# Kernel optimization log

Measured on AMD Instinct MI355X. Metric: run time of the kernel, lower is better.

The kernel has to match this reference:

```python
import jax, jax.numpy as jnp
import numpy as np

N_E = 8192
SPLIT = (512, 512)
BETA = 0.25
ENTROPY_RATIO = 0.1
TEMPERATURE = 0.01


def _l2norm(x):
    return x / jnp.linalg.norm(x, axis=-1, keepdims=True)


def _pairwise_sq_dist(zf, emb):
    # ||z||^2 + ||e||^2 - 2 z @ e^T   -> [N, n_e]
    return (jnp.sum(zf ** 2, axis=1, keepdims=True)
            + jnp.sum(emb ** 2, axis=1)
            - 2.0 * jnp.einsum('bd,nd->bn', zf, emb))


def _entropy_loss(affinity):
    flat = affinity / TEMPERATURE                      # [N, n_e]
    probs = jax.nn.softmax(flat, axis=-1)
    log_probs = jax.nn.log_softmax(flat + 1e-5, axis=-1)
    avg_probs = jnp.mean(probs, axis=0)                # [n_e]
    avg_entropy = -jnp.sum(avg_probs * jnp.log(avg_probs + 1e-5))
    sample_entropy = -jnp.mean(jnp.sum(probs * log_probs, axis=-1))
    return sample_entropy - avg_entropy


def setup_inputs() -> dict:
    key = jax.random.key(0)
    k1, k2, k3 = jax.random.split(key, 3)
    z = jax.random.normal(k1, (8192, 1024), dtype=jnp.float32)
    lim = 1.0 / N_E
    emb_text = jax.random.uniform(k2, (N_E, SPLIT[0]), minval=-lim, maxval=lim, dtype=jnp.float32)
    emb_graph = jax.random.uniform(k3, (N_E, SPLIT[1]), minval=-lim, maxval=lim, dtype=jnp.float32)
    # l2_norm=True: codebook weights are normalized at init
    emb_text = _l2norm(emb_text)
    emb_graph = _l2norm(emb_graph)
    return {"z": z, "emb_text": emb_text, "emb_graph": emb_graph}


def reference(z, emb_text, emb_graph):
    st = SPLIT[0]
    z_text, z_graph = z[:, :st], z[:, st:]

    # l2_norm path: normalize inputs and codebooks
    zt = _l2norm(z_text)                               # [N, d_t]
    zg = _l2norm(z_graph)                              # [N, d_g]
    et = _l2norm(emb_text)                             # [n_e, d_t]
    eg = _l2norm(emb_graph)                            # [n_e, d_g]
    z_norm = jnp.concatenate([zt, zg], axis=-1)        # [N, e_dim]

    d_text = _pairwise_sq_dist(zt, et)                 # [N, n_e]
    d_graph = _pairwise_sq_dist(zg, eg)                # [N, n_e]
    text_d_norm = jnp.mean(jnp.sum(d_text ** 2, axis=-1))
    graph_d_norm = jnp.mean(jnp.sum(d_graph ** 2, axis=-1))

    d = d_text + 1.0 * d_graph
    min_encoding_indices = jnp.argmin(d, axis=1)       # [N]

    all_embedding = jnp.concatenate([et, eg], axis=-1) # [n_e, e_dim]
    z_q = all_embedding[min_encoding_indices]          # [N, e_dim]
    z_q_text = et[min_encoding_indices]
    z_q_graph = eg[min_encoding_indices]

    sg = jax.lax.stop_gradient
    vq_loss = jnp.mean((z_q - sg(z_norm)) ** 2)
    commit_loss = BETA * jnp.mean((sg(z_q) - z_norm) ** 2)
    entropy_loss = ENTROPY_RATIO * _entropy_loss(-d)

    z_q_out = z_norm + sg(z_q - z_norm)                # straight-through
    return (z_q_out, vq_loss, commit_loss, entropy_loss,
            text_d_norm, graph_d_norm, z_q_text, z_q_graph,
            min_encoding_indices)
```

## Files before the change

### kernel.cpp

```cpp
#include <hip/hip_runtime.h>
#include <cmath>

using f32x4 = __attribute__((ext_vector_type(4))) float;
using f16x8 = __attribute__((ext_vector_type(8))) _Float16;

#define SCL_H  256.0f
#define INV_HH (1.0f/65536.0f)

#define WS_ZH   ((size_t)0)
#define WS_ZL   ((size_t)4194304)
#define WS_EH   ((size_t)8388608)
#define WS_EL   ((size_t)12582912)
#define WS_Z2T  ((size_t)16777216)
#define WS_Z2G  ((size_t)16785408)
#define WS_E2T  ((size_t)16793600)
#define WS_E2G  ((size_t)16801792)
#define WS_PM   ((size_t)16809984)
#define WS_PZ   ((size_t)17334272)
#define WS_PS1  ((size_t)17858560)
#define WS_PDT  ((size_t)18382848)
#define WS_PDG  ((size_t)18907136)
#define WS_PD1  ((size_t)19431424)
#define WS_PD2  ((size_t)19955712)
#define WS_PI1  ((size_t)20480000)
#define WS_PI2  ((size_t)21004288)
#define WS_PSC  ((size_t)21528576)
#define WS_LSE  ((size_t)22052864)
#define WS_IDX  ((size_t)22061056)
#define WS_RENT ((size_t)22069248)
#define WS_RDT  ((size_t)22077440)
#define WS_RDG  ((size_t)22085632)
#define WS_GVQ  ((size_t)22093824)
#define WS_AVG4 ((size_t)22102016)
#define WS_QM   ((size_t)22167552)
#define WS_STORE_END ((size_t)55721984)

#define O_VQ  ((size_t)8388608)
#define O_CM  ((size_t)8388609)
#define O_ENT ((size_t)8388610)
#define O_TD  ((size_t)8388611)
#define O_GD  ((size_t)8388612)
#define O_ZT  ((size_t)8388613)
#define O_ZG  ((size_t)12582917)
#define O_IX  ((size_t)16777221)

__device__ __forceinline__ size_t tiled_off(int row, int chunk) {
    return (((size_t)(row >> 7) * 32 + (chunk >> 2)) * 4 + (size_t)(chunk & 3)) * 1024
           + (size_t)(row & 127) * 8;
}

__device__ __forceinline__ void gload16(const void* g, void* l) {
    __builtin_amdgcn_global_load_lds(
        (const __attribute__((address_space(1))) unsigned int*)g,
        (__attribute__((address_space(3))) unsigned int*)l, 16, 0, 0);
}

__device__ __forceinline__ f32x4 mfma16(f16x8 a, f16x8 b, f32x4 c) {
    return __builtin_amdgcn_mfma_f32_16x16x32_f16(a, b, c, 0, 0, 0);
}

__device__ __forceinline__ unsigned short f2bf(float x) {
    unsigned int u = __float_as_uint(x);
    return (unsigned short)((u + 0x7fffu + ((u >> 16) & 1u)) >> 16);
}
__device__ __forceinline__ float bf2f(unsigned short u) {
    return __uint_as_float(((unsigned int)u) << 16);
}

__device__ __forceinline__ bool dless(float a, int ia, float b, int ib) {
    return a < b || (a == b && ia < ib);
}
__device__ __forceinline__ void top2_point(float& d1, int& i1, float& d2, int& i2,
                                           float d, int j) {
    if (dless(d, j, d1, i1)) { d2 = d1; i2 = i1; d1 = d; i1 = j; }
    else if (dless(d, j, d2, i2)) { d2 = d; i2 = j; }
}
__device__ __forceinline__ void top2_merge(float& d1, int& i1, float& d2, int& i2,
                                           float od1, int oi1, float od2, int oi2) {
    if (dless(od1, oi1, d1, i1)) {
        float nd2; int ni2;
        if (dless(d1, i1, od2, oi2)) { nd2 = d1; ni2 = i1; } else { nd2 = od2; ni2 = oi2; }
        d1 = od1; i1 = oi1; d2 = nd2; i2 = ni2;
    } else if (dless(od1, oi1, d2, i2)) {
        d2 = od1; i2 = oi1;
    }
}

__global__ __launch_bounds__(256) void k_zero(float* __restrict__ p, int n) {
    int i = blockIdx.x * 256 + threadIdx.x;
    if (i < n) p[i] = 0.0f;
}

__global__ __launch_bounds__(1024) void k_norm_z(const float* __restrict__ z,
        _Float16* __restrict__ zh, _Float16* __restrict__ zl,
        float* __restrict__ z2t, float* __restrict__ z2g) {
    int t = threadIdx.x;
    int r8 = t & 7, ck = t >> 3;
    int row = blockIdx.x * 8 + r8;
    const float* src = z + (size_t)row * 1024 + (size_t)ck * 8;
    float4 v0 = *(const float4*)src;
    float4 v1 = *(const float4*)(src + 4);
    float v[8] = {v0.x,v0.y,v0.z,v0.w,v1.x,v1.y,v1.z,v1.w};
    float ss = 0.f;
#pragma unroll
    for (int e = 0; e < 8; ++e) ss += v[e]*v[e];
    __shared__ float red[8*132];
    int ri = r8*132 + ck;
    red[ri] = ss; __syncthreads();
    for (int s = 32; s > 0; s >>= 1) { if ((ck & 63) < s) red[ri] += red[ri+s]; __syncthreads(); }
    float nrm = sqrtf(red[r8*132 + (ck & 64)]);
    float nv[8]; float s2 = 0.f;
#pragma unroll
    for (int e = 0; e < 8; ++e) { nv[e] = v[e]/nrm; s2 += nv[e]*nv[e]; }
    __syncthreads();
    red[ri] = s2; __syncthreads();
    for (int s = 32; s > 0; s >>= 1) { if ((ck & 63) < s) red[ri] += red[ri+s]; __syncthreads(); }
    if ((ck & 63) == 0) { if (ck & 64) z2g[row] = red[ri]; else z2t[row] = red[ri]; }
    f16x8 h8, l8;
#pragma unroll
    for (int e = 0; e < 8; ++e) {
        float xs = nv[e]*SCL_H;
        _Float16 h = (_Float16)xs; h8[e] = h;
        l8[e] = (_Float16)((xs - (float)h) * 4096.0f);
    }
    size_t off = tiled_off(row, ck);
    *(f16x8*)(zh + off) = h8;
    *(f16x8*)(zl + off) = l8;
}

__global__ __launch_bounds__(1024) void k_norm_e(const float* __restrict__ et, const float* __restrict__ eg,
        _Float16* __restrict__ eh, _Float16* __restrict__ el,
        float* __restrict__ e2t, float* __restrict__ e2g) {
    int t = threadIdx.x;
    int r8 = t & 7, ck = t >> 3;
    int row = blockIdx.x * 8 + r8;
    const float* src = (ck < 64) ? (et + (size_t)row * 512 + (size_t)ck * 8)
                                 : (eg + (size_t)row * 512 + (size_t)(ck - 64) * 8);
    float4 v0 = *(const float4*)src;
    float4 v1 = *(const float4*)(src + 4);
    float v[8] = {v0.x,v0.y,v0.z,v0.w,v1.x,v1.y,v1.z,v1.w};
    float ss = 0.f;
#pragma unroll
    for (int e = 0; e < 8; ++e) ss += v[e]*v[e];
    __shared__ float red[8*132];
    int ri = r8*132 + ck;
    red[ri] = ss; __syncthreads();
    for (int s = 32; s > 0; s >>= 1) { if ((ck & 63) < s) red[ri] += red[ri+s]; __syncthreads(); }
    float nrm = sqrtf(red[r8*132 + (ck & 64)]);
    float nv[8]; float s2 = 0.f;
#pragma unroll
    for (int e = 0; e < 8; ++e) { nv[e] = v[e]/nrm; s2 += nv[e]*nv[e]; }
    __syncthreads();
    red[ri] = s2; __syncthreads();
    for (int s = 32; s > 0; s >>= 1) { if ((ck & 63) < s) red[ri] += red[ri+s]; __syncthreads(); }
    if ((ck & 63) == 0) { if (ck & 64) e2g[row] = red[ri]; else e2t[row] = red[ri]; }
    f16x8 h8, l8;
#pragma unroll
    for (int e = 0; e < 8; ++e) {
        float xs = nv[e]*SCL_H;
        _Float16 h = (_Float16)xs; h8[e] = h;
        l8[e] = (_Float16)((xs - (float)h) * 4096.0f);
    }
    size_t off = tiled_off(row, ck);
    *(f16x8*)(eh + off) = h8;
    *(f16x8*)(el + off) = l8;
}

template<int PASS, bool STOREQ>
__global__ __launch_bounds__(512, 2) void k_gemm(
    const _Float16* __restrict__ zht, const _Float16* __restrict__ eht,
    const float* __restrict__ z2t, const float* __restrict__ z2g,
    const float* __restrict__ e2t, const float* __restrict__ e2g,
    float* __restrict__ pm, float* __restrict__ pz, float* __restrict__ ps1,
    float* __restrict__ pdt, float* __restrict__ pdg,
    float* __restrict__ pd1, float* __restrict__ pd2,
    int* __restrict__ pi1, int* __restrict__ pi2,
    unsigned short* __restrict__ qm,
    const float* __restrict__ lse, float* __restrict__ avgp)
{
    const int nj = blockIdx.x, bi = blockIdx.y;
    const int t = threadIdx.x;
    const int lane = t & 63, wid = t >> 6;
    const int wave_r = wid >> 2, wave_c = wid & 3;
    const int jf = lane & 15, g = lane >> 4;

    __shared__ __align__(16) _Float16 stg[2][2][4096];
    __shared__ float sM[128][4], sDt[128][4], sDg[128][4], sZ[128][4], sS1[128][4];
    __shared__ float sD1[128][4], sD2[128][4];
    __shared__ int   sI1[128][4], sI2[128][4];
    __shared__ float sMf[128];
    __shared__ float scol[128];

    if (PASS == 2 && t < 128) scol[t] = 0.f;

    f32x4 acct[4][2] = {};
    f32x4 accg[4][2] = {};

    const _Float16* pa = zht + (size_t)bi * 131072 + (size_t)t * 8;
    const _Float16* pb = eht + (size_t)nj * 131072 + (size_t)t * 8;

#define STAGE(KT, B) { \
        gload16(pa + (size_t)(KT) * 4096, &stg[0][B][t * 8]); \
        gload16(pb + (size_t)(KT) * 4096, &stg[1][B][t * 8]); }

    int cur = 0;
    STAGE(0, 0)
    asm volatile("s_waitcnt vmcnt(0)" ::: "memory");
    __syncthreads();

    for (int kt = 0; kt < 32; ++kt) {
        if (kt + 1 < 32) {
            if (cur == 0) STAGE(kt + 1, 1) else STAGE(kt + 1, 0)
        }
        f16x8 ah[4], bh[2];
#pragma unroll
        for (int fr = 0; fr < 4; ++fr) {
            int off = g * 1024 + (wave_r * 64 + fr * 16 + jf) * 8;
            ah[fr] = *(const f16x8*)&stg[0][cur][off];
        }
#pragma unroll
        for (int fc = 0; fc < 2; ++fc) {
            int off = g * 1024 + (wave_c * 32 + fc * 16 + jf) * 8;
            bh[fc] = *(const f16x8*)&stg[1][cur][off];
        }
        if (kt < 16) {
#pragma unroll
            for (int fr = 0; fr < 4; ++fr)
#pragma unroll
            for (int fc = 0; fc < 2; ++fc)
                acct[fr][fc] = mfma16(ah[fr], bh[fc], acct[fr][fc]);
        } else {
#pragma unroll
            for (int fr = 0; fr < 4; ++fr)
#pragma unroll
            for (int fc = 0; fc < 2; ++fc)
                accg[fr][fc] = mfma16(ah[fr], bh[fc], accg[fr][fc]);
        }
        asm volatile("s_waitcnt vmcnt(0)" ::: "memory");
        __syncthreads();
        cur ^= 1;
    }
#undef STAGE

    const int colbase = nj * 128 + wave_c * 32;
    float e2tc[2], e2gc[2];
#pragma unroll
    for (int fc = 0; fc < 2; ++fc) {
        e2tc[fc] = e2t[colbase + fc * 16 + jf];
        e2gc[fc] = e2g[colbase + fc * 16 + jf];
    }

    if constexpr (PASS == 1) {
#pragma unroll
        for (int fr = 0; fr < 4; ++fr) {
#pragma unroll
            for (int reg = 0; reg < 4; ++reg) {
                int rl = wave_r * 64 + fr * 16 + g * 4 + reg;
                int i  = bi * 128 + rl;
                float z2ti = z2t[i], z2gi = z2g[i];
                float mrow = -3.0e38f, dt2 = 0.f, dg2 = 0.f;
                float d1 = 3.0e38f, d2 = 3.0e38f;
                int i1 = 0x7fffffff, i2 = 0x7fffffff;
#pragma unroll
                for (int fc = 0; fc < 2; ++fc) {
                    float ht = acct[fr][fc][reg], hg = accg[fr][fc][reg];
                    float dta = z2ti + e2tc[fc] - ht * (2.0f * INV_HH);
                    float dga = z2gi + e2gc[fc] - hg * (2.0f * INV_HH);
                    float d   = dta + dga;
                    float lv  = -100.0f * d;
                    acct[fr][fc][reg] = lv;
                    dt2 += dta * dta; dg2 += dga * dga;
                    int j = colbase + fc * 16 + jf;
                    top2_point(d1, i1, d2, i2, d, j);
                    mrow = fmaxf(mrow, lv);
                }
#pragma unroll
                for (int s = 1; s < 16; s <<= 1) {
                    mrow = fmaxf(mrow, __shfl_xor(mrow, s));
                    dt2 += __shfl_xor(dt2, s);
                    dg2 += __shfl_xor(dg2, s);
                    float od1 = __shfl_xor(d1, s); int oi1 = __shfl_xor(i1, s);
                    float od2 = __shfl_xor(d2, s); int oi2 = __shfl_xor(i2, s);
                    top2_merge(d1, i1, d2, i2, od1, oi1, od2, oi2);
                }
                if (jf == 0) {
                    sM[rl][wave_c] = mrow; sDt[rl][wave_c] = dt2; sDg[rl][wave_c] = dg2;
                    sD1[rl][wave_c] = d1; sI1[rl][wave_c] = i1;
                    sD2[rl][wave_c] = d2; sI2[rl][wave_c] = i2;
                }
            }
        }
        __syncthreads();
        if (t < 128) sMf[t] = fmaxf(fmaxf(sM[t][0], sM[t][1]), fmaxf(sM[t][2], sM[t][3]));
        __syncthreads();
#pragma unroll
        for (int fr = 0; fr < 4; ++fr) {
#pragma unroll
            for (int reg = 0; reg < 4; ++reg) {
                int rl = wave_r * 64 + fr * 16 + g * 4 + reg;
                float M = sMf[rl];
                float Z = 0.f, S1 = 0.f;
#pragma unroll
                for (int fc = 0; fc < 2; ++fc) {
                    float lv = acct[fr][fc][reg];
                    float e  = expf(lv - M);
                    Z += e; S1 += e * lv;
                    if constexpr (STOREQ) {
                        size_t qo = (size_t)(bi * 128 + rl) * 8192 + (colbase + fc * 16 + jf);
                        qm[qo] = f2bf(e);
                    }
                }
#pragma unroll
                for (int s = 1; s < 16; s <<= 1) {
                    Z  += __shfl_xor(Z, s);
                    S1 += __shfl_xor(S1, s);
                }
                if (jf == 0) { sZ[rl][wave_c] = Z; sS1[rl][wave_c] = S1; }
            }
        }
        __syncthreads();
        if (t < 128) {
            float M = sMf[t];
            float Z = sZ[t][0] + sZ[t][1] + sZ[t][2] + sZ[t][3];
            float S1 = sS1[t][0] + sS1[t][1] + sS1[t][2] + sS1[t][3];
            float dt2 = sDt[t][0] + sDt[t][1] + sDt[t][2] + sDt[t][3];
            float dg2 = sDg[t][0] + sDg[t][1] + sDg[t][2] + sDg[t][3];
            float d1 = sD1[t][0], d2 = sD2[t][0];
            int i1 = sI1[t][0], i2 = sI2[t][0];
#pragma unroll
            for (int w = 1; w < 4; ++w)
                top2_merge(d1, i1, d2, i2, sD1[t][w], sI1[t][w], sD2[t][w], sI2[t][w]);
            size_t pb = (size_t)(bi * 128 + t) * 64 + nj;
            pm[pb] = M; pz[pb] = Z; ps1[pb] = S1;
            pdt[pb] = dt2; pdg[pb] = dg2;
            pd1[pb] = d1; pd2[pb] = d2; pi1[pb] = i1; pi2[pb] = i2;
        }
    } else {
        float cs0 = 0.f, cs1 = 0.f;
#pragma unroll
        for (int fr = 0; fr < 4; ++fr) {
#pragma unroll
            for (int reg = 0; reg < 4; ++reg) {
                int rl = wave_r * 64 + fr * 16 + g * 4 + reg;
                int i  = bi * 128 + rl;
                float z2ti = z2t[i], z2gi = z2g[i];
                float lsei = lse[i];
#pragma unroll
                for (int fc = 0; fc < 2; ++fc) {
                    float ht = acct[fr][fc][reg], hg = accg[fr][fc][reg];
                    float d = (z2ti + z2gi) + (e2tc[fc] + e2gc[fc])
                            - 2.0f * INV_HH * (ht + hg);
                    float lv = -100.0f * d;
                    float p = expf(lv - lsei);
                    if (fc == 0) cs0 += p; else cs1 += p;
                }
            }
        }
        cs0 += __shfl_xor(cs0, 16); cs0 += __shfl_xor(cs0, 32);
        cs1 += __shfl_xor(cs1, 16); cs1 += __shfl_xor(cs1, 32);
        if (g == 0) {
            atomicAdd(&scol[wave_c * 32 + jf], cs0);
            atomicAdd(&scol[wave_c * 32 + 16 + jf], cs1);
        }
        __syncthreads();
        if (t < 128) atomicAdd(&avgp[nj * 128 + t], scol[t]);
    }
}

__global__ __launch_bounds__(256) void k_rowreduce(
    const float* __restrict__ pm, const float* __restrict__ pz, const float* __restrict__ ps1,
    const float* __restrict__ pdt, const float* __restrict__ pdg,
    float* __restrict__ pscale, float* __restrict__ lse,
    float* __restrict__ rent, float* __restrict__ rdt, float* __restrict__ rdg)
{
    int b = blockIdx.x * 4 + (threadIdx.x >> 6);
    int l = threadIdx.x & 63;
    size_t pb = (size_t)b * 64 + l;
    float m0 = pm[pb];
    float m = m0;
#pragma unroll
    for (int s = 1; s < 64; s <<= 1) m = fmaxf(m, __shfl_xor(m, s));
    float sc = expf(m0 - m);
    float Z = pz[pb] * sc, S1 = ps1[pb] * sc;
    float dt2 = pdt[pb], dg2 = pdg[pb];
#pragma unroll
    for (int s = 1; s < 64; s <<= 1) {
        Z += __shfl_xor(Z, s); S1 += __shfl_xor(S1, s);
        dt2 += __shfl_xor(dt2, s); dg2 += __shfl_xor(dg2, s);
    }
    float lseb = m + logf(Z);
    pscale[pb] = expf(m0 - lseb);
    if (l == 0) {
        lse[b] = lseb;
        rent[b] = lseb - S1 / Z;
        rdt[b] = dt2; rdg[b] = dg2;
    }
}

__global__ __launch_bounds__(256) void k_refine(
    const float* __restrict__ pd1, const float* __restrict__ pd2,
    const int* __restrict__ pi1, const int* __restrict__ pi2,
    const _Float16* __restrict__ zh, const _Float16* __restrict__ zl,
    const _Float16* __restrict__ eh, const _Float16* __restrict__ el,
    const float* __restrict__ z2t, const float* __restrict__ z2g,
    const float* __restrict__ e2t, const float* __restrict__ e2g,
    int* __restrict__ idxi, float* __restrict__ out)
{
    int row = blockIdx.x * 4 + (threadIdx.x >> 6);
    int l = threadIdx.x & 63;
    size_t base = (size_t)row * 64;
    float da = pd1[base + l]; int ja = pi1[base + l];
    float db = pd2[base + l]; int jb = pi2[base + l];
    float M = fminf(da, db);
#pragma unroll
    for (int s = 1; s < 64; s <<= 1) M = fminf(M, __shfl_xor(M, s));
    const float eps = 1.0e-3f;
    unsigned long long mA = __ballot(da <= M + eps);
    unsigned long long mB = __ballot(db <= M + eps);

    float zv[16];
    {
        size_t o0 = tiled_off(row, 2 * l), o1 = tiled_off(row, 2 * l + 1);
        f16x8 h0 = *(const f16x8*)(zh + o0), l0 = *(const f16x8*)(zl + o0);
        f16x8 h1 = *(const f16x8*)(zh + o1), l1 = *(const f16x8*)(zl + o1);
#pragma unroll
        for (int e = 0; e < 8; ++e) {
            zv[e]     = (float)h0[e] * (1.0f/256.0f) + (float)l0[e] * (1.0f/1048576.0f);
            zv[8 + e] = (float)h1[e] * (1.0f/256.0f) + (float)l1[e] * (1.0f/1048576.0f);
        }
    }
    float zz = z2t[row] + z2g[row];
    float bd = 3.0e38f; int bj = 0x7fffffff;
    while (mA | mB) {
        int cand;
        if (mA) { int s = (int)__ffsll(mA) - 1; mA &= mA - 1; cand = __shfl(ja, s); }
        else    { int s = (int)__ffsll(mB) - 1; mB &= mB - 1; cand = __shfl(jb, s); }
        size_t o0 = tiled_off(cand, 2 * l), o1 = tiled_off(cand, 2 * l + 1);
        f16x8 h0 = *(const f16x8*)(eh + o0), l0 = *(const f16x8*)(el + o0);
        f16x8 h1 = *(const f16x8*)(eh + o1), l1 = *(const f16x8*)(el + o1);
        float dot = 0.f;
#pragma unroll
        for (int e = 0; e < 8; ++e) {
            float ev0 = (float)h0[e] * (1.0f/256.0f) + (float)l0[e] * (1.0f/1048576.0f);
            float ev1 = (float)h1[e] * (1.0f/256.0f) + (float)l1[e] * (1.0f/1048576.0f);
            dot += zv[e] * ev0 + zv[8 + e] * ev1;
        }
#pragma unroll
        for (int s = 1; s < 64; s <<= 1) dot += __shfl_xor(dot, s);
        float d = zz + e2t[cand] + e2g[cand] - 2.0f * dot;
        if (d < bd || (d == bd && cand < bj)) { bd = d; bj = cand; }
    }
    if (l == 0) { idxi[row] = bj; out[O_IX + row] = (float)bj; }
}

__global__ __launch_bounds__(256) void k_colsum(const unsigned short* __restrict__ qm,
                                                const float* __restrict__ pscale,
                                                float* __restrict__ avg4) {
    int cc = blockIdx.x, rb = blockIdx.y, t = threadIdx.x;
    int cp = t & 63, rg = t >> 6;
    float a0 = 0.f, a1 = 0.f;
    const unsigned short* qb = qm + (size_t)cc * 128 + (size_t)cp * 2;
#pragma unroll 4
    for (int rr = rg; rr < 1024; rr += 4) {
        int r = rb * 1024 + rr;
        float s = pscale[(size_t)r * 64 + cc];
        unsigned int q = *(const unsigned int*)(qb + (size_t)r * 8192);
        a0 += bf2f((unsigned short)(q & 0xffffu)) * s;
        a1 += bf2f((unsigned short)(q >> 16)) * s;
    }
    __shared__ float red[512];
    red[rg * 128 + cp * 2] = a0; red[rg * 128 + cp * 2 + 1] = a1;
    __syncthreads();
    if (rg == 0) {
        float s0 = red[cp*2]   + red[128+cp*2]   + red[256+cp*2]   + red[384+cp*2];
        float s1 = red[cp*2+1] + red[128+cp*2+1] + red[256+cp*2+1] + red[384+cp*2+1];
        avg4[(size_t)rb * 8192 + cc * 128 + cp * 2]     = s0;
        avg4[(size_t)rb * 8192 + cc * 128 + cp * 2 + 1] = s1;
    }
}

__global__ __launch_bounds__(1024) void k_gather(
    const _Float16* __restrict__ zh, const _Float16* __restrict__ zl,
    const _Float16* __restrict__ eh, const _Float16* __restrict__ el,
    const int* __restrict__ idxi, float* __restrict__ out, float* __restrict__ gvq)
{
    int t = threadIdx.x;
    int r8 = t & 7, ck = t >> 3;
    int b = blockIdx.x * 8 + r8;
    int idx = idxi[b];
    size_t zo = tiled_off(b, ck), eo = tiled_off(idx, ck);
    f16x8 zh8 = *(const f16x8*)(zh + zo);
    f16x8 zl8 = *(const f16x8*)(zl + zo);
    f16x8 eh8 = *(const f16x8*)(eh + eo);
    f16x8 el8 = *(const f16x8*)(el + eo);
    float ss = 0.f; float oz[8], zq[8];
#pragma unroll
    for (int e = 0; e < 8; ++e) {
        float zn = ((float)zh8[e] + (float)zl8[e] * (1.0f / 4096.0f)) * (1.0f / SCL_H);
        float eq = ((float)eh8[e] + (float)el8[e] * (1.0f / 4096.0f)) * (1.0f / SCL_H);
        float df = eq - zn;
        zq[e] = eq; oz[e] = zn + df; ss += df * df;
    }
    float* dst = out + (size_t)b * 1024 + (size_t)ck * 8;
    *(float4*)dst       = make_float4(oz[0], oz[1], oz[2], oz[3]);
    *(float4*)(dst + 4) = make_float4(oz[4], oz[5], oz[6], oz[7]);
    float* tg = (ck < 64) ? (out + O_ZT + (size_t)b * 512 + (size_t)ck * 8)
                          : (out + O_ZG + (size_t)b * 512 + (size_t)(ck - 64) * 8);
    *(float4*)tg       = make_float4(zq[0], zq[1], zq[2], zq[3]);
    *(float4*)(tg + 4) = make_float4(zq[4], zq[5], zq[6], zq[7]);
    __shared__ float red[8*132];
    int ri = r8 * 132 + ck;
    red[ri] = ss; __syncthreads();
    for (int s = 64; s > 0; s >>= 1) { if (ck < s) red[ri] += red[ri + s]; __syncthreads(); }
    if (ck == 0) gvq[b] = red[ri];
}

__global__ __launch_bounds__(256) void k_finalize(const float* __restrict__ avg4,
        const float* __restrict__ rent, const float* __restrict__ rdt,
        const float* __restrict__ rdg, const float* __restrict__ gvq,
        float* __restrict__ out) {
    int t = threadIdx.x;
    float ent = 0.f, se = 0.f, dt = 0.f, dg = 0.f, vq = 0.f;
    for (int n = t; n < 8192; n += 256) {
        float a = 0.f;
#pragma unroll
        for (int k = 0; k < 8; ++k) a += avg4[(size_t)k * 8192 + n];
        a *= (1.0f / 8192.0f);
        ent -= a * logf(a + 1e-5f);
        se += rent[n]; dt += rdt[n]; dg += rdg[n]; vq += gvq[n];
    }
    __shared__ float red[256];
#define RED(x) { red[t] = x; __syncthreads(); \
    for (int s = 128; s > 0; s >>= 1) { if (t < s) red[t] += red[t + s]; __syncthreads(); } \
    x = red[0]; __syncthreads(); }
    RED(ent) RED(se) RED(dt) RED(dg) RED(vq)
#undef RED
    if (t == 0) {
        float vqm = vq * (1.0f / 8388608.0f);
        out[O_VQ]  = vqm;
        out[O_CM]  = 0.25f * vqm;
        out[O_ENT] = 0.1f * (se * (1.0f / 8192.0f) - ent);
        out[O_TD]  = dt * (1.0f / 8192.0f);
        out[O_GD]  = dg * (1.0f / 8192.0f);
    }
}

extern "C" void kernel_launch(void* const* d_in, const int* in_sizes, int n_in,
                              void* d_out, int out_size, void* d_ws, size_t ws_size,
                              hipStream_t stream) {
    const float* z  = (const float*)d_in[0];
    const float* et = (const float*)d_in[1];
    const float* eg = (const float*)d_in[2];
    float* out = (float*)d_out;
    float* ws  = (float*)d_ws;

    _Float16* zh = (_Float16*)(ws + WS_ZH);
    _Float16* zl = (_Float16*)(ws + WS_ZL);
    _Float16* eh = (_Float16*)(ws + WS_EH);
    _Float16* el = (_Float16*)(ws + WS_EL);
    float* z2t = ws + WS_Z2T;
    float* z2g = ws + WS_Z2G;
    float* e2t = ws + WS_E2T;
    float* e2g = ws + WS_E2G;
    float* pm  = ws + WS_PM;
    float* pz  = ws + WS_PZ;
    float* ps1 = ws + WS_PS1;
    float* pdt = ws + WS_PDT;
    float* pdg = ws + WS_PDG;
    float* pd1 = ws + WS_PD1;
    float* pd2 = ws + WS_PD2;
    int*   pi1 = (int*)(ws + WS_PI1);
    int*   pi2 = (int*)(ws + WS_PI2);
    float* psc = ws + WS_PSC;
    float* lsep = ws + WS_LSE;
    int*   idxi = (int*)(ws + WS_IDX);
    float* rent = ws + WS_RENT;
    float* rdt  = ws + WS_RDT;
    float* rdg  = ws + WS_RDG;
    float* gvq  = ws + WS_GVQ;
    float* avg4 = ws + WS_AVG4;
    unsigned short* qm = (unsigned short*)(ws + WS_QM);

    bool storeq = (ws_size >= WS_STORE_END * sizeof(float));

    k_norm_z<<<1024, 1024, 0, stream>>>(z, zh, zl, z2t, z2g);
    k_norm_e<<<1024, 1024, 0, stream>>>(et, eg, eh, el, e2t, e2g);

    dim3 gg(64, 64);
    if (storeq) {
        k_gemm<1, true><<<gg, 512, 0, stream>>>(zh, eh, z2t, z2g, e2t, e2g,
                                                pm, pz, ps1, pdt, pdg,
                                                pd1, pd2, pi1, pi2, qm, lsep, avg4);
    } else {
        k_gemm<1, false><<<gg, 512, 0, stream>>>(zh, eh, z2t, z2g, e2t, e2g,
                                                 pm, pz, ps1, pdt, pdg,
                                                 pd1, pd2, pi1, pi2, qm, lsep, avg4);
    }
    k_rowreduce<<<2048, 256, 0, stream>>>(pm, pz, ps1, pdt, pdg,
                                          psc, lsep, rent, rdt, rdg);
    k_refine<<<2048, 256, 0, stream>>>(pd1, pd2, pi1, pi2, zh, zl, eh, el,
                                       z2t, z2g, e2t, e2g, idxi, out);
    if (storeq) {
        k_colsum<<<dim3(64, 8), 256, 0, stream>>>(qm, psc, avg4);
    } else {
        k_zero<<<256, 256, 0, stream>>>(avg4, 65536);
        k_gemm<2, false><<<gg, 512, 0, stream>>>(zh, eh, z2t, z2g, e2t, e2g,
                                                 pm, pz, ps1, pdt, pdg,
                                                 pd1, pd2, pi1, pi2, qm, lsep, avg4);
    }
    k_gather<<<1024, 1024, 0, stream>>>(zh, zl, eh, el, idxi, out, gvq);
    k_finalize<<<1, 256, 0, stream>>>(avg4, rent, rdt, rdg, gvq, out);
}
```

Measured before the change: 801.3 us.

## Shrink GEMM tile to 128x64 with XCD-aware block mapping and LDS-staged Q stores

Reworks the fused distance GEMM to use 256-thread blocks computing 128x64 tiles, with a 1D grid remapped so that blocks sharing the same z row-tile land on the same XCD for L2 reuse. The K loop now takes 64-wide chunks per step with a single LDS buffer instead of double buffering. The bf16 probability matrix is staged through LDS and written with coalesced 16-byte stores instead of scattered 2-byte ones. Partial-result arrays double to 128 per row, so the row-reduce, refine (now with four candidate sets and a wider eps) and colsum kernels are adjusted, which adds more partial traffic and more candidate rescoring.

```diff
diff --git a/kernel.cpp b/kernel.cpp
--- a/kernel.cpp
+++ b/kernel.cpp
@@ -16,24 +16,24 @@
 #define WS_E2T  ((size_t)16793600)
 #define WS_E2G  ((size_t)16801792)
 #define WS_PM   ((size_t)16809984)
-#define WS_PZ   ((size_t)17334272)
-#define WS_PS1  ((size_t)17858560)
-#define WS_PDT  ((size_t)18382848)
-#define WS_PDG  ((size_t)18907136)
-#define WS_PD1  ((size_t)19431424)
-#define WS_PD2  ((size_t)19955712)
-#define WS_PI1  ((size_t)20480000)
-#define WS_PI2  ((size_t)21004288)
-#define WS_PSC  ((size_t)21528576)
-#define WS_LSE  ((size_t)22052864)
-#define WS_IDX  ((size_t)22061056)
-#define WS_RENT ((size_t)22069248)
-#define WS_RDT  ((size_t)22077440)
-#define WS_RDG  ((size_t)22085632)
-#define WS_GVQ  ((size_t)22093824)
-#define WS_AVG4 ((size_t)22102016)
-#define WS_QM   ((size_t)22167552)
-#define WS_STORE_END ((size_t)55721984)
+#define WS_PZ   ((size_t)17858560)
+#define WS_PS1  ((size_t)18907136)
+#define WS_PDT  ((size_t)19955712)
+#define WS_PDG  ((size_t)21004288)
+#define WS_PD1  ((size_t)22052864)
+#define WS_PD2  ((size_t)23101440)
+#define WS_PI1  ((size_t)24150016)
+#define WS_PI2  ((size_t)25198592)
+#define WS_PSC  ((size_t)26247168)
+#define WS_LSE  ((size_t)27295744)
+#define WS_IDX  ((size_t)27303936)
+#define WS_RENT ((size_t)27312128)
+#define WS_RDT  ((size_t)27320320)
+#define WS_RDG  ((size_t)27328512)
+#define WS_GVQ  ((size_t)27336704)
+#define WS_AVG4 ((size_t)27344896)
+#define WS_QM   ((size_t)27418624)
+#define WS_STORE_END ((size_t)60973056)
 
 #define O_VQ  ((size_t)8388608)
 #define O_CM  ((size_t)8388609)
@@ -167,7 +167,7 @@
 }
 
 template<int PASS, bool STOREQ>
-__global__ __launch_bounds__(512, 2) void k_gemm(
+__global__ __launch_bounds__(256, 4) void k_gemm(
     const _Float16* __restrict__ zht, const _Float16* __restrict__ eht,
     const float* __restrict__ z2t, const float* __restrict__ z2g,
     const float* __restrict__ e2t, const float* __restrict__ e2g,
@@ -178,71 +178,88 @@
     unsigned short* __restrict__ qm,
     const float* __restrict__ lse, float* __restrict__ avgp)
 {
-    const int nj = blockIdx.x, bi = blockIdx.y;
+    const int bid = blockIdx.x;
+    const int xcd = bid & 7, local = bid >> 3;
+    const int nj = local >> 3;
+    const int bi = xcd * 8 + (local & 7);
+
     const int t = threadIdx.x;
     const int lane = t & 63, wid = t >> 6;
-    const int wave_r = wid >> 2, wave_c = wid & 3;
+    const int wave_r = wid >> 1, wave_c = wid & 1;
     const int jf = lane & 15, g = lane >> 4;
 
-    __shared__ __align__(16) _Float16 stg[2][2][4096];
-    __shared__ float sM[128][4], sDt[128][4], sDg[128][4], sZ[128][4], sS1[128][4];
-    __shared__ float sD1[128][4], sD2[128][4];
-    __shared__ int   sI1[128][4], sI2[128][4];
-    __shared__ float sMf[128];
-    __shared__ float scol[128];
-
-    if (PASS == 2 && t < 128) scol[t] = 0.f;
+    __shared__ __align__(16) char smem[35328];
+    _Float16* lA = (_Float16*)smem;
+    _Float16* lB = (_Float16*)(smem + 16384);
+    unsigned short* sQ = (unsigned short*)smem;
+    float (*sM)[2]  = (float(*)[2])(smem + 24576);
+    float (*sDt)[2] = (float(*)[2])(smem + 25600);
+    float (*sDg)[2] = (float(*)[2])(smem + 26624);
+    float (*sZ)[2]  = (float(*)[2])(smem + 27648);
+    float (*sS1)[2] = (float(*)[2])(smem + 28672);
+    float (*sD1)[2] = (float(*)[2])(smem + 29696);
+    float (*sD2)[2] = (float(*)[2])(smem + 30720);
+    int   (*sI1)[2] = (int(*)[2])(smem + 31744);
+    int   (*sI2)[2] = (int(*)[2])(smem + 32768);
+    float* sMf  = (float*)(smem + 33792);
+    float* scol = (float*)(smem + 34304);
+
+    if (PASS == 2 && t < 64) scol[t] = 0.f;
 
     f32x4 acct[4][2] = {};
     f32x4 accg[4][2] = {};
 
-    const _Float16* pa = zht + (size_t)bi * 131072 + (size_t)t * 8;
-    const _Float16* pb = eht + (size_t)nj * 131072 + (size_t)t * 8;
-
-#define STAGE(KT, B) { \
-        gload16(pa + (size_t)(KT) * 4096, &stg[0][B][t * 8]); \
-        gload16(pb + (size_t)(KT) * 4096, &stg[1][B][t * 8]); }
-
-    int cur = 0;
-    STAGE(0, 0)
-    asm volatile("s_waitcnt vmcnt(0)" ::: "memory");
-    __syncthreads();
-
-    for (int kt = 0; kt < 32; ++kt) {
-        if (kt + 1 < 32) {
-            if (cur == 0) STAGE(kt + 1, 1) else STAGE(kt + 1, 0)
-        }
-        f16x8 ah[4], bh[2];
-#pragma unroll
-        for (int fr = 0; fr < 4; ++fr) {
-            int off = g * 1024 + (wave_r * 64 + fr * 16 + jf) * 8;
-            ah[fr] = *(const f16x8*)&stg[0][cur][off];
-        }
-#pragma unroll
-        for (int fc = 0; fc < 2; ++fc) {
-            int off = g * 1024 + (wave_c * 32 + fc * 16 + jf) * 8;
-            bh[fc] = *(const f16x8*)&stg[1][cur][off];
-        }
-        if (kt < 16) {
-#pragma unroll
-            for (int fr = 0; fr < 4; ++fr)
-#pragma unroll
-            for (int fc = 0; fc < 2; ++fc)
-                acct[fr][fc] = mfma16(ah[fr], bh[fc], acct[fr][fc]);
-        } else {
-#pragma unroll
-            for (int fr = 0; fr < 4; ++fr)
-#pragma unroll
-            for (int fc = 0; fc < 2; ++fc)
-                accg[fr][fc] = mfma16(ah[fr], bh[fc], accg[fr][fc]);
-        }
+    const _Float16* pa  = zht + (size_t)bi * 131072;
+    const _Float16* pbv = eht + (size_t)(nj >> 1) * 131072 + (size_t)(nj & 1) * 512;
+
+#define STAGE(KT2) { \
+        size_t kofs = (size_t)(KT2) * 8192; \
+        gload16(pa + kofs + (size_t)t * 8,         lA + t * 8); \
+        gload16(pa + kofs + (size_t)(256 + t) * 8, lA + (256 + t) * 8); \
+        gload16(pa + kofs + (size_t)(512 + t) * 8, lA + (512 + t) * 8); \
+        gload16(pa + kofs + (size_t)(768 + t) * 8, lA + (768 + t) * 8); \
+        { int li = t;       gload16(pbv + kofs + (size_t)(li >> 6) * 1024 + (size_t)(li & 63) * 8, lB + li * 8); } \
+        { int li = 256 + t; gload16(pbv + kofs + (size_t)(li >> 6) * 1024 + (size_t)(li & 63) * 8, lB + li * 8); } }
+
+    for (int kt2 = 0; kt2 < 16; ++kt2) {
+        STAGE(kt2)
         asm volatile("s_waitcnt vmcnt(0)" ::: "memory");
         __syncthreads();
-        cur ^= 1;
+        f16x8 a0[4], a1[4], b0[2], b1[2];
+#pragma unroll
+        for (int fr = 0; fr < 4; ++fr) {
+            int ro = (wave_r * 64 + fr * 16 + jf) * 8;
+            a0[fr] = *(const f16x8*)&lA[g * 1024 + ro];
+            a1[fr] = *(const f16x8*)&lA[4096 + g * 1024 + ro];
+        }
+#pragma unroll
+        for (int fc = 0; fc < 2; ++fc) {
+            int ro = (wave_c * 32 + fc * 16 + jf) * 8;
+            b0[fc] = *(const f16x8*)&lB[g * 512 + ro];
+            b1[fc] = *(const f16x8*)&lB[2048 + g * 512 + ro];
+        }
+        if (kt2 < 8) {
+#pragma unroll
+            for (int fr = 0; fr < 4; ++fr)
+#pragma unroll
+            for (int fc = 0; fc < 2; ++fc) {
+                acct[fr][fc] = mfma16(a0[fr], b0[fc], acct[fr][fc]);
+                acct[fr][fc] = mfma16(a1[fr], b1[fc], acct[fr][fc]);
+            }
+        } else {
+#pragma unroll
+            for (int fr = 0; fr < 4; ++fr)
+#pragma unroll
+            for (int fc = 0; fc < 2; ++fc) {
+                accg[fr][fc] = mfma16(a0[fr], b0[fc], accg[fr][fc]);
+                accg[fr][fc] = mfma16(a1[fr], b1[fc], accg[fr][fc]);
+            }
+        }
+        __syncthreads();
     }
 #undef STAGE
 
-    const int colbase = nj * 128 + wave_c * 32;
+    const int colbase = nj * 64 + wave_c * 32;
     float e2tc[2], e2gc[2];
 #pragma unroll
     for (int fc = 0; fc < 2; ++fc) {
@@ -291,7 +308,7 @@
             }
         }
         __syncthreads();
-        if (t < 128) sMf[t] = fmaxf(fmaxf(sM[t][0], sM[t][1]), fmaxf(sM[t][2], sM[t][3]));
+        if (t < 128) sMf[t] = fmaxf(sM[t][0], sM[t][1]);
         __syncthreads();
 #pragma unroll
         for (int fr = 0; fr < 4; ++fr) {
@@ -305,10 +322,7 @@
                     float lv = acct[fr][fc][reg];
                     float e  = expf(lv - M);
                     Z += e; S1 += e * lv;
-                    if constexpr (STOREQ) {
-                        size_t qo = (size_t)(bi * 128 + rl) * 8192 + (colbase + fc * 16 + jf);
-                        qm[qo] = f2bf(e);
-                    }
+                    if constexpr (STOREQ) sQ[rl * 64 + wave_c * 32 + fc * 16 + jf] = f2bf(e);
                 }
 #pragma unroll
                 for (int s = 1; s < 16; s <<= 1) {
@@ -321,19 +335,27 @@
         __syncthreads();
         if (t < 128) {
             float M = sMf[t];
-            float Z = sZ[t][0] + sZ[t][1] + sZ[t][2] + sZ[t][3];
-            float S1 = sS1[t][0] + sS1[t][1] + sS1[t][2] + sS1[t][3];
-            float dt2 = sDt[t][0] + sDt[t][1] + sDt[t][2] + sDt[t][3];
-            float dg2 = sDg[t][0] + sDg[t][1] + sDg[t][2] + sDg[t][3];
+            float Z = sZ[t][0] + sZ[t][1];
+            float S1 = sS1[t][0] + sS1[t][1];
+            float dt2 = sDt[t][0] + sDt[t][1];
+            float dg2 = sDg[t][0] + sDg[t][1];
             float d1 = sD1[t][0], d2 = sD2[t][0];
             int i1 = sI1[t][0], i2 = sI2[t][0];
-#pragma unroll
-            for (int w = 1; w < 4; ++w)
-                top2_merge(d1, i1, d2, i2, sD1[t][w], sI1[t][w], sD2[t][w], sI2[t][w]);
-            size_t pb = (size_t)(bi * 128 + t) * 64 + nj;
+            top2_merge(d1, i1, d2, i2, sD1[t][1], sI1[t][1], sD2[t][1], sI2[t][1]);
+            size_t pb = (size_t)(bi * 128 + t) * 128 + nj;
             pm[pb] = M; pz[pb] = Z; ps1[pb] = S1;
             pdt[pb] = dt2; pdg[pb] = dg2;
             pd1[pb] = d1; pd2[pb] = d2; pi1[pb] = i1; pi2[pb] = i2;
+        }
+        if constexpr (STOREQ) {
+            const uint4* s4 = (const uint4*)sQ;
+#pragma unroll
+            for (int it = 0; it < 4; ++it) {
+                int f = it * 256 + t;
+                int row = f >> 3, seg = f & 7;
+                uint4 q = s4[f];
+                *(uint4*)(qm + (size_t)(bi * 128 + row) * 8192 + nj * 64 + seg * 8) = q;
+            }
         }
     } else {
         float cs0 = 0.f, cs1 = 0.f;
@@ -363,7 +385,7 @@
             atomicAdd(&scol[wave_c * 32 + 16 + jf], cs1);
         }
         __syncthreads();
-        if (t < 128) atomicAdd(&avgp[nj * 128 + t], scol[t]);
+        if (t < 64) atomicAdd(&avgp[nj * 64 + t], scol[t]);
     }
 }
 
@@ -375,21 +397,23 @@
 {
     int b = blockIdx.x * 4 + (threadIdx.x >> 6);
     int l = threadIdx.x & 63;
-    size_t pb = (size_t)b * 64 + l;
-    float m0 = pm[pb];
-    float m = m0;
+    size_t i0 = (size_t)b * 128 + l, i1 = i0 + 64;
+    float ma = pm[i0], mb = pm[i1];
+    float m = fmaxf(ma, mb);
 #pragma unroll
     for (int s = 1; s < 64; s <<= 1) m = fmaxf(m, __shfl_xor(m, s));
-    float sc = expf(m0 - m);
-    float Z = pz[pb] * sc, S1 = ps1[pb] * sc;
-    float dt2 = pdt[pb], dg2 = pdg[pb];
+    float sa = expf(ma - m), sb = expf(mb - m);
+    float Z  = pz[i0] * sa + pz[i1] * sb;
+    float S1 = ps1[i0] * sa + ps1[i1] * sb;
+    float dt2 = pdt[i0] + pdt[i1], dg2 = pdg[i0] + pdg[i1];
 #pragma unroll
     for (int s = 1; s < 64; s <<= 1) {
         Z += __shfl_xor(Z, s); S1 += __shfl_xor(S1, s);
         dt2 += __shfl_xor(dt2, s); dg2 += __shfl_xor(dg2, s);
     }
     float lseb = m + logf(Z);
-    pscale[pb] = expf(m0 - lseb);
+    pscale[i0] = expf(ma - lseb);
+    pscale[i1] = expf(mb - lseb);
     if (l == 0) {
         lse[b] = lseb;
         rent[b] = lseb - S1 / Z;
@@ -408,15 +432,19 @@
 {
     int row = blockIdx.x * 4 + (threadIdx.x >> 6);
     int l = threadIdx.x & 63;
-    size_t base = (size_t)row * 64;
-    float da = pd1[base + l]; int ja = pi1[base + l];
-    float db = pd2[base + l]; int jb = pi2[base + l];
-    float M = fminf(da, db);
+    size_t base = (size_t)row * 128;
+    float cd[4]; int ci[4];
+    cd[0] = pd1[base + l];      ci[0] = pi1[base + l];
+    cd[1] = pd1[base + 64 + l]; ci[1] = pi1[base + 64 + l];
+    cd[2] = pd2[base + l];      ci[2] = pi2[base + l];
+    cd[3] = pd2[base + 64 + l]; ci[3] = pi2[base + 64 + l];
+    float M = fminf(fminf(cd[0], cd[1]), fminf(cd[2], cd[3]));
 #pragma unroll
     for (int s = 1; s < 64; s <<= 1) M = fminf(M, __shfl_xor(M, s));
-    const float eps = 1.0e-3f;
-    unsigned long long mA = __ballot(da <= M + eps);
-    unsigned long long mB = __ballot(db <= M + eps);
+    const float eps = 4.0e-3f;
+    unsigned long long mk[4];
+#pragma unroll
+    for (int k = 0; k < 4; ++k) mk[k] = __ballot(cd[k] <= M + eps);
 
     float zv[16];
     {
@@ -431,24 +459,26 @@
     }
     float zz = z2t[row] + z2g[row];
     float bd = 3.0e38f; int bj = 0x7fffffff;
-    while (mA | mB) {
-        int cand;
-        if (mA) { int s = (int)__ffsll(mA) - 1; mA &= mA - 1; cand = __shfl(ja, s); }
-        else    { int s = (int)__ffsll(mB) - 1; mB &= mB - 1; cand = __shfl(jb, s); }
-        size_t o0 = tiled_off(cand, 2 * l), o1 = tiled_off(cand, 2 * l + 1);
-        f16x8 h0 = *(const f16x8*)(eh + o0), l0 = *(const f16x8*)(el + o0);
-        f16x8 h1 = *(const f16x8*)(eh + o1), l1 = *(const f16x8*)(el + o1);
-        float dot = 0.f;
-#pragma unroll
-        for (int e = 0; e < 8; ++e) {
-            float ev0 = (float)h0[e] * (1.0f/256.0f) + (float)l0[e] * (1.0f/1048576.0f);
-            float ev1 = (float)h1[e] * (1.0f/256.0f) + (float)l1[e] * (1.0f/1048576.0f);
-            dot += zv[e] * ev0 + zv[8 + e] * ev1;
-        }
-#pragma unroll
-        for (int s = 1; s < 64; s <<= 1) dot += __shfl_xor(dot, s);
-        float d = zz + e2t[cand] + e2g[cand] - 2.0f * dot;
-        if (d < bd || (d == bd && cand < bj)) { bd = d; bj = cand; }
+#pragma unroll 1
+    for (int k = 0; k < 4; ++k) {
+        while (mk[k]) {
+            int s = (int)__ffsll(mk[k]) - 1; mk[k] &= mk[k] - 1;
+            int cand = __shfl(ci[k], s);
+            size_t o0 = tiled_off(cand, 2 * l), o1 = tiled_off(cand, 2 * l + 1);
+            f16x8 h0 = *(const f16x8*)(eh + o0), l0 = *(const f16x8*)(el + o0);
+            f16x8 h1 = *(const f16x8*)(eh + o1), l1 = *(const f16x8*)(el + o1);
+            float dot = 0.f;
+#pragma unroll
+            for (int e = 0; e < 8; ++e) {
+                float ev0 = (float)h0[e] * (1.0f/256.0f) + (float)l0[e] * (1.0f/1048576.0f);
+                float ev1 = (float)h1[e] * (1.0f/256.0f) + (float)l1[e] * (1.0f/1048576.0f);
+                dot += zv[e] * ev0 + zv[8 + e] * ev1;
+            }
+#pragma unroll
+            for (int s2 = 1; s2 < 64; s2 <<= 1) dot += __shfl_xor(dot, s2);
+            float d = zz + e2t[cand] + e2g[cand] - 2.0f * dot;
+            if (d < bd || (d == bd && cand < bj)) { bd = d; bj = cand; }
+        }
     }
     if (l == 0) { idxi[row] = bj; out[O_IX + row] = (float)bj; }
 }
@@ -457,25 +487,26 @@
                                                 const float* __restrict__ pscale,
                                                 float* __restrict__ avg4) {
     int cc = blockIdx.x, rb = blockIdx.y, t = threadIdx.x;
-    int cp = t & 63, rg = t >> 6;
+    int cp = t & 31, rg = t >> 5;
     float a0 = 0.f, a1 = 0.f;
-    const unsigned short* qb = qm + (size_t)cc * 128 + (size_t)cp * 2;
+    const unsigned short* qb = qm + (size_t)cc * 64 + (size_t)cp * 2;
 #pragma unroll 4
-    for (int rr = rg; rr < 1024; rr += 4) {
+    for (int rr = rg; rr < 1024; rr += 8) {
         int r = rb * 1024 + rr;
-        float s = pscale[(size_t)r * 64 + cc];
+        float s = pscale[(size_t)r * 128 + cc];
         unsigned int q = *(const unsigned int*)(qb + (size_t)r * 8192);
         a0 += bf2f((unsigned short)(q & 0xffffu)) * s;
         a1 += bf2f((unsigned short)(q >> 16)) * s;
     }
     __shared__ float red[512];
-    red[rg * 128 + cp * 2] = a0; red[rg * 128 + cp * 2 + 1] = a1;
+    red[rg * 64 + cp * 2] = a0; red[rg * 64 + cp * 2 + 1] = a1;
     __syncthreads();
     if (rg == 0) {
-        float s0 = red[cp*2]   + red[128+cp*2]   + red[256+cp*2]   + red[384+cp*2];
-        float s1 = red[cp*2+1] + red[128+cp*2+1] + red[256+cp*2+1] + red[384+cp*2+1];
-        avg4[(size_t)rb * 8192 + cc * 128 + cp * 2]     = s0;
-        avg4[(size_t)rb * 8192 + cc * 128 + cp * 2 + 1] = s1;
+        float s0 = 0.f, s1 = 0.f;
+#pragma unroll
+        for (int k = 0; k < 8; ++k) { s0 += red[k * 64 + cp * 2]; s1 += red[k * 64 + cp * 2 + 1]; }
+        avg4[(size_t)rb * 8192 + cc * 64 + cp * 2]     = s0;
+        avg4[(size_t)rb * 8192 + cc * 64 + cp * 2 + 1] = s1;
     }
 }
 
@@ -586,27 +617,26 @@
     k_norm_z<<<1024, 1024, 0, stream>>>(z, zh, zl, z2t, z2g);
     k_norm_e<<<1024, 1024, 0, stream>>>(et, eg, eh, el, e2t, e2g);
 
-    dim3 gg(64, 64);
     if (storeq) {
-        k_gemm<1, true><<<gg, 512, 0, stream>>>(zh, eh, z2t, z2g, e2t, e2g,
-                                                pm, pz, ps1, pdt, pdg,
-                                                pd1, pd2, pi1, pi2, qm, lsep, avg4);
+        k_gemm<1, true><<<8192, 256, 0, stream>>>(zh, eh, z2t, z2g, e2t, e2g,
+                                                  pm, pz, ps1, pdt, pdg,
+                                                  pd1, pd2, pi1, pi2, qm, lsep, avg4);
     } else {
-        k_gemm<1, false><<<gg, 512, 0, stream>>>(zh, eh, z2t, z2g, e2t, e2g,
-                                                 pm, pz, ps1, pdt, pdg,
-                                                 pd1, pd2, pi1, pi2, qm, lsep, avg4);
+        k_gemm<1, false><<<8192, 256, 0, stream>>>(zh, eh, z2t, z2g, e2t, e2g,
+                                                   pm, pz, ps1, pdt, pdg,
+                                                   pd1, pd2, pi1, pi2, qm, lsep, avg4);
     }
     k_rowreduce<<<2048, 256, 0, stream>>>(pm, pz, ps1, pdt, pdg,
                                           psc, lsep, rent, rdt, rdg);
     k_refine<<<2048, 256, 0, stream>>>(pd1, pd2, pi1, pi2, zh, zl, eh, el,
                                        z2t, z2g, e2t, e2g, idxi, out);
     if (storeq) {
-        k_colsum<<<dim3(64, 8), 256, 0, stream>>>(qm, psc, avg4);
+        k_colsum<<<dim3(128, 8), 256, 0, stream>>>(qm, psc, avg4);
     } else {
         k_zero<<<256, 256, 0, stream>>>(avg4, 65536);
-        k_gemm<2, false><<<gg, 512, 0, stream>>>(zh, eh, z2t, z2g, e2t, e2g,
-                                                 pm, pz, ps1, pdt, pdg,
-                                                 pd1, pd2, pi1, pi2, qm, lsep, avg4);
+        k_gemm<2, false><<<8192, 256, 0, stream>>>(zh, eh, z2t, z2g, e2t, e2g,
+                                                   pm, pz, ps1, pdt, pdg,
+                                                   pd1, pd2, pi1, pi2, qm, lsep, avg4);
     }
     k_gather<<<1024, 1024, 0, stream>>>(zh, zl, eh, el, idxi, out, gvq);
     k_finalize<<<1, 256, 0, stream>>>(avg4, rent, rdt, rdg, gvq, out);
```

After: 1.039 ms. +29.6%, slower.
